# Kernel optimization log

Measured on AMD Instinct MI355X. Metric: run time of the kernel, lower is better.

Reference implementation:

```python
import jax, jax.numpy as jnp
import numpy as np

EMBED_DIM = 1024
NUM_HEADS = 16
HEAD_DIM = EMBED_DIM // NUM_HEADS


def setup_inputs() -> dict:
    key = jax.random.key(0)
    ks = jax.random.split(key, 9)
    B, S, D = 4, 2048, EMBED_DIM
    s = 1.0 / np.sqrt(D)
    return {
        "x": jax.random.normal(ks[0], (B, S, D), dtype=jnp.float32),
        "Wq": jax.random.normal(ks[1], (D, D), dtype=jnp.float32) * s,
        "bq": jnp.zeros((D,), dtype=jnp.float32),
        "Wk": jax.random.normal(ks[2], (D, D), dtype=jnp.float32) * s,
        "bk": jnp.zeros((D,), dtype=jnp.float32),
        "Wv": jax.random.normal(ks[3], (D, D), dtype=jnp.float32) * s,
        "bv": jnp.zeros((D,), dtype=jnp.float32),
        "Wo": jax.random.normal(ks[4], (D, D), dtype=jnp.float32) * s,
        "bo": jnp.zeros((D,), dtype=jnp.float32),
    }


def reference(x, Wq, bq, Wk, bk, Wv, bv, Wo, bo):
    B, S, D = x.shape
    H, Hd = NUM_HEADS, HEAD_DIM

    def proj(W, b):
        # [B,S,D] -> [B,H,S,Hd]
        y = jnp.einsum('bsd,de->bse', x, W) + b
        return y.reshape(B, S, H, Hd).transpose(0, 2, 1, 3)

    q = proj(Wq, bq)
    k = proj(Wk, bk)
    v = proj(Wv, bv)

    scale = 1.0 / jnp.sqrt(jnp.asarray(Hd, dtype=x.dtype))
    scores = jnp.einsum('bhqd,bhkd->bhqk', q, k) * scale  # [B,H,S,S]
    attn = jax.nn.softmax(scores, axis=-1)
    # dropout is identity in eval/inference mode
    heads = jnp.einsum('bhqk,bhkd->bhqd', attn, v)  # [B,H,S,Hd]
    heads = heads.transpose(0, 2, 1, 3).reshape(B, S, D)
    z = jnp.einsum('bsd,de->bse', heads, Wo) + bo
    return z
```

## Files before the change

kernel.cpp:

```cpp
#include <hip/hip_runtime.h>


typedef __attribute__((ext_vector_type(8))) short bf16x8;
typedef __attribute__((ext_vector_type(4))) float f32x4;

#define MFMA16 __builtin_amdgcn_mfma_f32_16x16x32_bf16

__device__ __forceinline__ unsigned short f2bf(float f) {
  unsigned int u = __float_as_uint(f);
  u += 0x7fff + ((u >> 16) & 1);
  return (unsigned short)(u >> 16);
}

__device__ __forceinline__ void gl2l16(const unsigned short* g, unsigned short* l) {
  __builtin_amdgcn_global_load_lds((const __attribute__((address_space(1))) void*)g,
                                   (__attribute__((address_space(3))) void*)l, 16, 0, 0);
}

__global__ __launch_bounds__(256) void k_convert_x(const float* __restrict__ x,
                                                   unsigned short* __restrict__ xb) {
  int i = (blockIdx.x * 256 + threadIdx.x) * 4;
  float4 v = *(const float4*)(x + i);
  ushort4 u;
  u.x = f2bf(v.x); u.y = f2bf(v.y); u.z = f2bf(v.z); u.w = f2bf(v.w);
  *(ushort4*)(xb + i) = u;
}

__global__ __launch_bounds__(256) void k_transpose_w(const float* w0, const float* w1,
                                                     const float* w2, const float* w3,
                                                     unsigned short* o0, unsigned short* o1,
                                                     unsigned short* o2, unsigned short* o3) {
  const float* W = blockIdx.z == 0 ? w0 : blockIdx.z == 1 ? w1 : blockIdx.z == 2 ? w2 : w3;
  unsigned short* O = blockIdx.z == 0 ? o0 : blockIdx.z == 1 ? o1 : blockIdx.z == 2 ? o2 : o3;
  __shared__ float t[32][33];
  int e0 = blockIdx.x * 32, d0 = blockIdx.y * 32;
  #pragma unroll
  for (int i = 0; i < 4; i++)
    t[threadIdx.y + i * 8][threadIdx.x] = W[(d0 + threadIdx.y + i * 8) * 1024 + e0 + threadIdx.x];
  __syncthreads();
  #pragma unroll
  for (int i = 0; i < 4; i++)
    O[(e0 + threadIdx.y + i * 8) * 1024 + d0 + threadIdx.x] = f2bf(t[threadIdx.x][threadIdx.y + i * 8]);
}

__global__ __launch_bounds__(256) void gemm_qkv(const unsigned short* __restrict__ A,
                                                const unsigned short* __restrict__ BtQ,
                                                const unsigned short* __restrict__ BtK,
                                                const unsigned short* __restrict__ BtV,
                                                const float* __restrict__ biq,
                                                const float* __restrict__ bik,
                                                const float* __restrict__ biv,
                                                unsigned short* __restrict__ oq,
                                                unsigned short* __restrict__ ok,
                                                unsigned short* __restrict__ ov,
                                                float qscale) {
  const int z = blockIdx.z;
  const unsigned short* Bt = z == 0 ? BtQ : z == 1 ? BtK : BtV;
  const float* bias = z == 0 ? biq : z == 1 ? bik : biv;
  unsigned short* out = z == 0 ? oq : z == 1 ? ok : ov;
  const float scale = z == 0 ? qscale : 1.0f;

  const int tid = threadIdx.x;
  const int lane = tid & 63, w = tid >> 6;
  const int wr = (w >> 1) * 64, wc = (w & 1) * 64;
  const int fm = lane & 15, quad = lane >> 4;
  const int bm0 = blockIdx.y * 128, bn0 = blockIdx.x * 128;

  __shared__ unsigned short As[128 * 32];
  __shared__ unsigned short Bs[128 * 32];

  f32x4 acc[4][4] = {};

  const int srow = lane >> 2;
  const int sswz = ((lane & 3) ^ (srow & 3)) * 8;
  const unsigned short* gA = A + (size_t)(bm0 + w * 32 + srow) * 1024 + sswz;
  const unsigned short* gB = Bt + (size_t)(bn0 + w * 32 + srow) * 1024 + sswz;
  unsigned short* lA = As + w * 1024;
  unsigned short* lB = Bs + w * 1024;

  const int cswz = (fm & 3);

  for (int kb = 0; kb < 1024; kb += 32) {
    gl2l16(gA + kb, lA);
    gl2l16(gA + kb + 16 * 1024, lA + 512);
    gl2l16(gB + kb, lB);
    gl2l16(gB + kb + 16 * 1024, lB + 512);
    __syncthreads();
    bf16x8 af[4], bfr[4];
    #pragma unroll
    for (int mt = 0; mt < 4; mt++)
      af[mt] = *(const bf16x8*)&As[(wr + mt * 16 + fm) * 32 + ((quad ^ cswz) * 8)];
    #pragma unroll
    for (int nt = 0; nt < 4; nt++)
      bfr[nt] = *(const bf16x8*)&Bs[(wc + nt * 16 + fm) * 32 + ((quad ^ cswz) * 8)];
    #pragma unroll
    for (int mt = 0; mt < 4; mt++)
      #pragma unroll
      for (int nt = 0; nt < 4; nt++)
        acc[mt][nt] = MFMA16(af[mt], bfr[nt], acc[mt][nt], 0, 0, 0);
    __syncthreads();
  }

  float bv[4];
  #pragma unroll
  for (int nt = 0; nt < 4; nt++) bv[nt] = bias[bn0 + wc + nt * 16 + fm];

  #pragma unroll
  for (int mt = 0; mt < 4; mt++) {
    #pragma unroll
    for (int nt = 0; nt < 4; nt++) {
      #pragma unroll
      for (int r = 0; r < 4; r++) {
        int row = bm0 + wr + mt * 16 + quad * 4 + r;
        int col = bn0 + wc + nt * 16 + fm;
        float v = (acc[mt][nt][r] + bv[nt]) * scale;
        int b = row >> 11, s = row & 2047, h = col >> 6, hd = col & 63;
        if (z < 2)
          out[(((b << 4) + h) * 2048 + s) * 64 + hd] = f2bf(v);
        else
          out[(((b << 4) + h) * 64 + hd) * 2048 + s] = f2bf(v);
      }
    }
  }
}

__global__ __launch_bounds__(256) void gemm_out(const unsigned short* __restrict__ A,
                                                const unsigned short* __restrict__ Bt,
                                                const float* __restrict__ bias,
                                                float* __restrict__ out) {
  const int tid = threadIdx.x;
  const int lane = tid & 63, w = tid >> 6;
  const int wr = (w >> 1) * 64, wc = (w & 1) * 64;
  const int fm = lane & 15, quad = lane >> 4;
  const int bm0 = blockIdx.y * 128, bn0 = blockIdx.x * 128;

  __shared__ unsigned short As[128 * 32];
  __shared__ unsigned short Bs[128 * 32];

  f32x4 acc[4][4] = {};

  const int srow = lane >> 2;
  const int sswz = ((lane & 3) ^ (srow & 3)) * 8;
  const unsigned short* gA = A + (size_t)(bm0 + w * 32 + srow) * 1024 + sswz;
  const unsigned short* gB = Bt + (size_t)(bn0 + w * 32 + srow) * 1024 + sswz;
  unsigned short* lA = As + w * 1024;
  unsigned short* lB = Bs + w * 1024;

  const int cswz = (fm & 3);

  for (int kb = 0; kb < 1024; kb += 32) {
    gl2l16(gA + kb, lA);
    gl2l16(gA + kb + 16 * 1024, lA + 512);
    gl2l16(gB + kb, lB);
    gl2l16(gB + kb + 16 * 1024, lB + 512);
    __syncthreads();
    bf16x8 af[4], bfr[4];
    #pragma unroll
    for (int mt = 0; mt < 4; mt++)
      af[mt] = *(const bf16x8*)&As[(wr + mt * 16 + fm) * 32 + ((quad ^ cswz) * 8)];
    #pragma unroll
    for (int nt = 0; nt < 4; nt++)
      bfr[nt] = *(const bf16x8*)&Bs[(wc + nt * 16 + fm) * 32 + ((quad ^ cswz) * 8)];
    #pragma unroll
    for (int mt = 0; mt < 4; mt++)
      #pragma unroll
      for (int nt = 0; nt < 4; nt++)
        acc[mt][nt] = MFMA16(af[mt], bfr[nt], acc[mt][nt], 0, 0, 0);
    __syncthreads();
  }

  float bv[4];
  #pragma unroll
  for (int nt = 0; nt < 4; nt++) bv[nt] = bias[bn0 + wc + nt * 16 + fm];

  #pragma unroll
  for (int mt = 0; mt < 4; mt++)
    #pragma unroll
    for (int nt = 0; nt < 4; nt++)
      #pragma unroll
      for (int r = 0; r < 4; r++) {
        int row = bm0 + wr + mt * 16 + quad * 4 + r;
        int col = bn0 + wc + nt * 16 + fm;
        out[(size_t)row * 1024 + col] = acc[mt][nt][r] + bv[nt];
      }
}

__global__ __launch_bounds__(256) void k_attn(const unsigned short* __restrict__ q,
                                              const unsigned short* __restrict__ k,
                                              const unsigned short* __restrict__ vt,
                                              unsigned short* __restrict__ heads) {
  const int tid = threadIdx.x, lane = tid & 63, w = tid >> 6;
  const int fm = lane & 15, quad = lane >> 4, k0 = quad * 8;
  const int qt = blockIdx.x, bh = blockIdx.y;
  const int b = bh >> 4, h = bh & 15;
  const unsigned short* qg = q + (size_t)bh * 2048 * 64;
  const unsigned short* kg = k + (size_t)bh * 2048 * 64;
  const unsigned short* vg = vt + (size_t)bh * 64 * 2048;

  __shared__ unsigned short Ks[64 * 64];
  __shared__ unsigned short Vs[64 * 64];
  __shared__ unsigned short Ps[4][32 * 72];

  const int sr = lane >> 3;
  const int sswz = ((lane & 7) ^ sr) * 8;
  const unsigned short* gK = kg + (w * 16 + sr) * 64 + sswz;
  const unsigned short* gV = vg + (size_t)(w * 16 + sr) * 2048 + sswz;
  unsigned short* lK = Ks + w * 1024;
  unsigned short* lV = Vs + w * 1024;

  bf16x8 aq[2][2];
  #pragma unroll
  for (int mt = 0; mt < 2; mt++)
    #pragma unroll
    for (int kh = 0; kh < 2; kh++)
      aq[mt][kh] = *(const bf16x8*)&qg[(qt * 128 + w * 32 + mt * 16 + fm) * 64 + kh * 32 + k0];

  bf16x8 onesf;
  #pragma unroll
  for (int i = 0; i < 8; i++) onesf[i] = (short)0x3F80;

  f32x4 o[2][4] = {};
  f32x4 la[2] = {};
  const int fsw = fm & 7;

  for (int kb = 0; kb < 32; kb++) {
    __syncthreads();
    gl2l16(gK + kb * 4096, lK);
    gl2l16(gK + kb * 4096 + 512, lK + 512);
    gl2l16(gV + kb * 64, lV);
    gl2l16(gV + kb * 64 + 8 * 2048, lV + 512);
    __syncthreads();

    f32x4 s[2][4] = {};
    #pragma unroll
    for (int nt = 0; nt < 4; nt++) {
      #pragma unroll
      for (int kh = 0; kh < 2; kh++) {
        bf16x8 bK = *(const bf16x8*)&Ks[(nt * 16 + fm) * 64 + (((kh * 4 + quad) ^ fsw) * 8)];
        s[0][nt] = MFMA16(aq[0][kh], bK, s[0][nt], 0, 0, 0);
        s[1][nt] = MFMA16(aq[1][kh], bK, s[1][nt], 0, 0, 0);
      }
    }

    #pragma unroll
    for (int mt = 0; mt < 2; mt++)
      #pragma unroll
      for (int nt = 0; nt < 4; nt++)
        #pragma unroll
        for (int r = 0; r < 4; r++) {
          float p = __builtin_amdgcn_exp2f(s[mt][nt][r]);
          unsigned int t = __float_as_uint(p) + 0x8000u;
          Ps[w][(mt * 16 + quad * 4 + r) * 72 + nt * 16 + fm] = (unsigned short)(t >> 16);
        }

    #pragma unroll
    for (int ks = 0; ks < 2; ks++) {
      bf16x8 ap[2];
      #pragma unroll
      for (int mt = 0; mt < 2; mt++) {
        ap[mt] = *(const bf16x8*)&Ps[w][(mt * 16 + fm) * 72 + ks * 32 + k0];
        la[mt] = MFMA16(ap[mt], onesf, la[mt], 0, 0, 0);
      }
      #pragma unroll
      for (int nt = 0; nt < 4; nt++) {
        bf16x8 bV = *(const bf16x8*)&Vs[(nt * 16 + fm) * 64 + (((ks * 4 + quad) ^ fsw) * 8)];
        o[0][nt] = MFMA16(ap[0], bV, o[0][nt], 0, 0, 0);
        o[1][nt] = MFMA16(ap[1], bV, o[1][nt], 0, 0, 0);
      }
    }
  }

  #pragma unroll
  for (int mt = 0; mt < 2; mt++)
    #pragma unroll
    for (int r = 0; r < 4; r++) {
      float inv = 1.0f / la[mt][r];
      int srw = qt * 128 + w * 32 + mt * 16 + quad * 4 + r;
      #pragma unroll
      for (int nt = 0; nt < 4; nt++)
        heads[(size_t)(b * 2048 + srw) * 1024 + h * 64 + nt * 16 + fm] =
            f2bf(o[mt][nt][r] * inv);
    }
}

extern "C" void kernel_launch(void* const* d_in, const int* in_sizes, int n_in,
                              void* d_out, int out_size, void* d_ws, size_t ws_size,
                              hipStream_t stream) {
  const float* x  = (const float*)d_in[0];
  const float* Wq = (const float*)d_in[1];
  const float* bq = (const float*)d_in[2];
  const float* Wk = (const float*)d_in[3];
  const float* bk = (const float*)d_in[4];
  const float* Wv = (const float*)d_in[5];
  const float* bv = (const float*)d_in[6];
  const float* Wo = (const float*)d_in[7];
  const float* bo = (const float*)d_in[8];
  float* out = (float*)d_out;

  char* ws = (char*)d_ws;
  unsigned short* xb  = (unsigned short*)(ws);
  unsigned short* wtq = (unsigned short*)(ws + (16u << 20));
  unsigned short* wtk = (unsigned short*)(ws + (18u << 20));
  unsigned short* wtv = (unsigned short*)(ws + (20u << 20));
  unsigned short* wto = (unsigned short*)(ws + (22u << 20));
  unsigned short* qb  = (unsigned short*)(ws + (24u << 20));
  unsigned short* kb2 = (unsigned short*)(ws + (40u << 20));
  unsigned short* vtb = (unsigned short*)(ws + (56u << 20));
  unsigned short* hb  = (unsigned short*)(ws + (72u << 20));

  k_convert_x<<<8192, 256, 0, stream>>>(x, xb);
  k_transpose_w<<<dim3(32, 32, 4), dim3(32, 8), 0, stream>>>(Wq, Wk, Wv, Wo, wtq, wtk, wtv, wto);

  const float qscale = 0.125f * 1.44269504088896f;
  gemm_qkv<<<dim3(8, 64, 3), 256, 0, stream>>>(xb, wtq, wtk, wtv, bq, bk, bv,
                                               qb, kb2, vtb, qscale);

  k_attn<<<dim3(16, 64), 256, 0, stream>>>(qb, kb2, vtb, hb);

  gemm_out<<<dim3(8, 64), 256, 0, stream>>>(hb, wto, bo, out);
}
```

Baseline: 321.9 us.

## Double-buffer LDS tiles in GEMM and attention loops, reorder attention grid

```diff
diff --git a/kernel.cpp b/kernel.cpp
--- a/kernel.cpp
+++ b/kernel.cpp
@@ -41,6 +41,40 @@
   #pragma unroll
   for (int i = 0; i < 4; i++)
     O[(e0 + threadIdx.y + i * 8) * 1024 + d0 + threadIdx.x] = f2bf(t[threadIdx.x][threadIdx.y + i * 8]);
+}
+
+__device__ __forceinline__ void kloop_dbuf(const unsigned short* __restrict__ gA,
+                                           const unsigned short* __restrict__ gB,
+                                           unsigned short* As, unsigned short* Bs,
+                                           int w, int fm, int quad, int wr, int wc,
+                                           f32x4 (&acc)[4][4]) {
+  const int cswz8 = (quad ^ (fm & 3)) * 8;
+  unsigned short* lA = As + w * 1024;
+  unsigned short* lB = Bs + w * 1024;
+  gl2l16(gA, lA); gl2l16(gA + 16 * 1024, lA + 512);
+  gl2l16(gB, lB); gl2l16(gB + 16 * 1024, lB + 512);
+  for (int kb = 0; kb < 32; kb++) {
+    const int cur = (kb & 1) * 4096;
+    __syncthreads();
+    if (kb < 31) {
+      const int nxt = 4096 - cur;
+      const int off = (kb + 1) * 32;
+      gl2l16(gA + off, lA + nxt); gl2l16(gA + off + 16 * 1024, lA + nxt + 512);
+      gl2l16(gB + off, lB + nxt); gl2l16(gB + off + 16 * 1024, lB + nxt + 512);
+    }
+    bf16x8 af[4], bfr[4];
+    #pragma unroll
+    for (int mt = 0; mt < 4; mt++)
+      af[mt] = *(const bf16x8*)&As[cur + (wr + mt * 16 + fm) * 32 + cswz8];
+    #pragma unroll
+    for (int nt = 0; nt < 4; nt++)
+      bfr[nt] = *(const bf16x8*)&Bs[cur + (wc + nt * 16 + fm) * 32 + cswz8];
+    #pragma unroll
+    for (int mt = 0; mt < 4; mt++)
+      #pragma unroll
+      for (int nt = 0; nt < 4; nt++)
+        acc[mt][nt] = MFMA16(af[mt], bfr[nt], acc[mt][nt], 0, 0, 0);
+  }
 }
 
 __global__ __launch_bounds__(256) void gemm_qkv(const unsigned short* __restrict__ A,
@@ -66,8 +100,8 @@
   const int fm = lane & 15, quad = lane >> 4;
   const int bm0 = blockIdx.y * 128, bn0 = blockIdx.x * 128;
 
-  __shared__ unsigned short As[128 * 32];
-  __shared__ unsigned short Bs[128 * 32];
+  __shared__ unsigned short As[2 * 128 * 32];
+  __shared__ unsigned short Bs[2 * 128 * 32];
 
   f32x4 acc[4][4] = {};
 
@@ -75,31 +109,8 @@
   const int sswz = ((lane & 3) ^ (srow & 3)) * 8;
   const unsigned short* gA = A + (size_t)(bm0 + w * 32 + srow) * 1024 + sswz;
   const unsigned short* gB = Bt + (size_t)(bn0 + w * 32 + srow) * 1024 + sswz;
-  unsigned short* lA = As + w * 1024;
-  unsigned short* lB = Bs + w * 1024;
-
-  const int cswz = (fm & 3);
-
-  for (int kb = 0; kb < 1024; kb += 32) {
-    gl2l16(gA + kb, lA);
-    gl2l16(gA + kb + 16 * 1024, lA + 512);
-    gl2l16(gB + kb, lB);
-    gl2l16(gB + kb + 16 * 1024, lB + 512);
-    __syncthreads();
-    bf16x8 af[4], bfr[4];
-    #pragma unroll
-    for (int mt = 0; mt < 4; mt++)
-      af[mt] = *(const bf16x8*)&As[(wr + mt * 16 + fm) * 32 + ((quad ^ cswz) * 8)];
-    #pragma unroll
-    for (int nt = 0; nt < 4; nt++)
-      bfr[nt] = *(const bf16x8*)&Bs[(wc + nt * 16 + fm) * 32 + ((quad ^ cswz) * 8)];
-    #pragma unroll
-    for (int mt = 0; mt < 4; mt++)
-      #pragma unroll
-      for (int nt = 0; nt < 4; nt++)
-        acc[mt][nt] = MFMA16(af[mt], bfr[nt], acc[mt][nt], 0, 0, 0);
-    __syncthreads();
-  }
+
+  kloop_dbuf(gA, gB, As, Bs, w, fm, quad, wr, wc, acc);
 
   float bv[4];
   #pragma unroll
@@ -134,8 +145,8 @@
   const int fm = lane & 15, quad = lane >> 4;
   const int bm0 = blockIdx.y * 128, bn0 = blockIdx.x * 128;
 
-  __shared__ unsigned short As[128 * 32];
-  __shared__ unsigned short Bs[128 * 32];
+  __shared__ unsigned short As[2 * 128 * 32];
+  __shared__ unsigned short Bs[2 * 128 * 32];
 
   f32x4 acc[4][4] = {};
 
@@ -143,31 +154,8 @@
   const int sswz = ((lane & 3) ^ (srow & 3)) * 8;
   const unsigned short* gA = A + (size_t)(bm0 + w * 32 + srow) * 1024 + sswz;
   const unsigned short* gB = Bt + (size_t)(bn0 + w * 32 + srow) * 1024 + sswz;
-  unsigned short* lA = As + w * 1024;
-  unsigned short* lB = Bs + w * 1024;
-
-  const int cswz = (fm & 3);
-
-  for (int kb = 0; kb < 1024; kb += 32) {
-    gl2l16(gA + kb, lA);
-    gl2l16(gA + kb + 16 * 1024, lA + 512);
-    gl2l16(gB + kb, lB);
-    gl2l16(gB + kb + 16 * 1024, lB + 512);
-    __syncthreads();
-    bf16x8 af[4], bfr[4];
-    #pragma unroll
-    for (int mt = 0; mt < 4; mt++)
-      af[mt] = *(const bf16x8*)&As[(wr + mt * 16 + fm) * 32 + ((quad ^ cswz) * 8)];
-    #pragma unroll
-    for (int nt = 0; nt < 4; nt++)
-      bfr[nt] = *(const bf16x8*)&Bs[(wc + nt * 16 + fm) * 32 + ((quad ^ cswz) * 8)];
-    #pragma unroll
-    for (int mt = 0; mt < 4; mt++)
-      #pragma unroll
-      for (int nt = 0; nt < 4; nt++)
-        acc[mt][nt] = MFMA16(af[mt], bfr[nt], acc[mt][nt], 0, 0, 0);
-    __syncthreads();
-  }
+
+  kloop_dbuf(gA, gB, As, Bs, w, fm, quad, wr, wc, acc);
 
   float bv[4];
   #pragma unroll
@@ -191,14 +179,14 @@
                                               unsigned short* __restrict__ heads) {
   const int tid = threadIdx.x, lane = tid & 63, w = tid >> 6;
   const int fm = lane & 15, quad = lane >> 4, k0 = quad * 8;
-  const int qt = blockIdx.x, bh = blockIdx.y;
+  const int bh = blockIdx.x, qt = blockIdx.y;
   const int b = bh >> 4, h = bh & 15;
   const unsigned short* qg = q + (size_t)bh * 2048 * 64;
   const unsigned short* kg = k + (size_t)bh * 2048 * 64;
   const unsigned short* vg = vt + (size_t)bh * 64 * 2048;
 
-  __shared__ unsigned short Ks[64 * 64];
-  __shared__ unsigned short Vs[64 * 64];
+  __shared__ unsigned short Ks[2 * 64 * 64];
+  __shared__ unsigned short Vs[2 * 64 * 64];
   __shared__ unsigned short Ps[4][32 * 72];
 
   const int sr = lane >> 3;
@@ -223,20 +211,26 @@
   f32x4 la[2] = {};
   const int fsw = fm & 7;
 
+  gl2l16(gK, lK); gl2l16(gK + 512, lK + 512);
+  gl2l16(gV, lV); gl2l16(gV + 8 * 2048, lV + 512);
+
   for (int kb = 0; kb < 32; kb++) {
+    const int cur = (kb & 1) * 4096;
     __syncthreads();
-    gl2l16(gK + kb * 4096, lK);
-    gl2l16(gK + kb * 4096 + 512, lK + 512);
-    gl2l16(gV + kb * 64, lV);
-    gl2l16(gV + kb * 64 + 8 * 2048, lV + 512);
-    __syncthreads();
+    if (kb < 31) {
+      const int nxt = 4096 - cur;
+      gl2l16(gK + (kb + 1) * 4096, lK + nxt);
+      gl2l16(gK + (kb + 1) * 4096 + 512, lK + nxt + 512);
+      gl2l16(gV + (kb + 1) * 64, lV + nxt);
+      gl2l16(gV + (kb + 1) * 64 + 8 * 2048, lV + nxt + 512);
+    }
 
     f32x4 s[2][4] = {};
     #pragma unroll
     for (int nt = 0; nt < 4; nt++) {
       #pragma unroll
       for (int kh = 0; kh < 2; kh++) {
-        bf16x8 bK = *(const bf16x8*)&Ks[(nt * 16 + fm) * 64 + (((kh * 4 + quad) ^ fsw) * 8)];
+        bf16x8 bK = *(const bf16x8*)&Ks[cur + (nt * 16 + fm) * 64 + (((kh * 4 + quad) ^ fsw) * 8)];
         s[0][nt] = MFMA16(aq[0][kh], bK, s[0][nt], 0, 0, 0);
         s[1][nt] = MFMA16(aq[1][kh], bK, s[1][nt], 0, 0, 0);
       }
@@ -263,7 +257,7 @@
       }
       #pragma unroll
       for (int nt = 0; nt < 4; nt++) {
-        bf16x8 bV = *(const bf16x8*)&Vs[(nt * 16 + fm) * 64 + (((ks * 4 + quad) ^ fsw) * 8)];
+        bf16x8 bV = *(const bf16x8*)&Vs[cur + (nt * 16 + fm) * 64 + (((ks * 4 + quad) ^ fsw) * 8)];
         o[0][nt] = MFMA16(ap[0], bV, o[0][nt], 0, 0, 0);
         o[1][nt] = MFMA16(ap[1], bV, o[1][nt], 0, 0, 0);
       }
@@ -315,7 +309,7 @@
   gemm_qkv<<<dim3(8, 64, 3), 256, 0, stream>>>(xb, wtq, wtk, wtv, bq, bk, bv,
                                                qb, kb2, vtb, qscale);
 
-  k_attn<<<dim3(16, 64), 256, 0, stream>>>(qb, kb2, vtb, hb);
+  k_attn<<<dim3(64, 16), 256, 0, stream>>>(qb, kb2, vtb, hb);
 
   gemm_out<<<dim3(8, 64), 256, 0, stream>>>(hb, wto, bo, out);
 }
```

Result: slower. 347.1 us (+7.8%).
